# Performance work log

Hardware: AMD Instinct MI355X
Metric: run time of the kernel (lower is better)

## Reference

```python
import jax, jax.numpy as jnp
import numpy as np


def setup_inputs() -> dict:
    key = jax.random.key(0)
    k1, k2, k3, k4, k5, k6 = jax.random.split(key, 6)
    bs, sl, max_nw, dim_vtw, dim_hidden = 32, 1024, 16, 64, 128
    xw = jax.random.normal(k1, (bs, sl, max_nw, dim_vtw), dtype=jnp.float32)
    # xn: [bs, sl, ns+1]; only last column (word length, in [1, max_nw]) is used
    xn = jax.random.randint(k2, (bs, sl, 4), 1, max_nw + 1)
    s = 1.0 / np.sqrt(dim_hidden)
    W_ih = jax.random.uniform(k3, (4 * dim_hidden, dim_vtw), minval=-s, maxval=s, dtype=jnp.float32)
    W_hh = jax.random.uniform(k4, (4 * dim_hidden, dim_hidden), minval=-s, maxval=s, dtype=jnp.float32)
    b_ih = jax.random.uniform(k5, (4 * dim_hidden,), minval=-s, maxval=s, dtype=jnp.float32)
    b_hh = jax.random.uniform(k6, (4 * dim_hidden,), minval=-s, maxval=s, dtype=jnp.float32)
    return {"xw": xw, "xn": xn, "W_ih": W_ih, "W_hh": W_hh, "b_ih": b_ih, "b_hh": b_hh}


def reference(xw, xn, W_ih, W_hh, b_ih, b_hh):
    # Vectorized equivalent of the original per-group loop: run the LSTM over
    # the full max_nw timesteps for every (b, s) position (LSTM is causal, so
    # the hidden state after nw steps equals running only the first nw steps),
    # then gather h at t = length-1 per position.
    bs, sl, T, D = xw.shape
    H = W_hh.shape[1]
    N = bs * sl
    x = xw.reshape(N, T, D)
    lengths = xn[:, :, -1].reshape(N)
    # Precompute input contributions to all 4 gates: [T, N, 4H]
    x_gates = jnp.einsum('ntd,gd->tng', x, W_ih) + (b_ih + b_hh)

    def step(carry, xg):
        h, c = carry
        gates = xg + h @ W_hh.T  # [N, 4H]
        i, f, g, o = jnp.split(gates, 4, axis=-1)
        i = jax.nn.sigmoid(i)
        f = jax.nn.sigmoid(f)
        g = jnp.tanh(g)
        o = jax.nn.sigmoid(o)
        c = f * c + i * g
        h = o * jnp.tanh(c)
        return (h, c), h

    init = (jnp.zeros((N, H), xw.dtype), jnp.zeros((N, H), xw.dtype))
    _, hs = jax.lax.scan(step, init, x_gates)  # hs: [T, N, H]
    hs = jnp.swapaxes(hs, 0, 1)  # [N, T, H]
    idx = jnp.clip(lengths - 1, 0, T - 1)
    h_final = jnp.take_along_axis(hs, idx[:, None, None], axis=1)[:, 0]  # [N, H]
    return h_final.reshape(bs, sl, H)
```

## Files before the change

kernel.cpp:

```cpp
#include <hip/hip_runtime.h>
#include <math.h>

#define T_STEPS 16
#define DIM_X 64
#define DIM_H 128
#define DIM_K 192
#define NPACK 512
#define MSEQ 64
#define NTHREADS 512
#define LDK 200
#define PREP_THREADS 256
#define PACK_ITEMS (NPACK * DIM_K)
#define PACK_BLOCKS (PACK_ITEMS / PREP_THREADS)

typedef __attribute__((ext_vector_type(8))) short bf16x8;
typedef __attribute__((ext_vector_type(4))) float f32x4;

__device__ __forceinline__ float fsigmoid(float x) {
    return 1.0f / (1.0f + __expf(-x));
}
__device__ __forceinline__ float ftanh_(float x) {
    float a = fabsf(x);
    float e = __expf(2.0f * a);
    float r = 1.0f - 2.0f / (e + 1.0f);
    return copysignf(r, x);
}
__device__ __forceinline__ unsigned short bf16_rn(float x) {
    unsigned int b = __float_as_uint(x);
    b += 0x7FFFu + ((b >> 16) & 1u);
    return (unsigned short)(b >> 16);
}
__device__ __forceinline__ float bf16_to_f(unsigned short u) {
    return __uint_as_float(((unsigned int)u) << 16);
}

__global__ __launch_bounds__(PREP_THREADS)
void prep(const float* __restrict__ W_ih, const float* __restrict__ W_hh,
          const float* __restrict__ b_ih, const float* __restrict__ b_hh,
          const int* __restrict__ xn, int N,
          unsigned short* __restrict__ Whi, unsigned short* __restrict__ Wlo,
          float* __restrict__ bsum, int* __restrict__ list, int* __restrict__ ctr) {
    const int b = blockIdx.x;
    const int tid = threadIdx.x;
    if (b < PACK_BLOCKS) {
        int i = b * PREP_THREADS + tid;
        int p = i / DIM_K, k = i % DIM_K;
        int g = (p >> 4) & 3;
        int unit = ((p >> 6) << 4) + (p & 15);
        int r = g * DIM_H + unit;
        float v = (k < DIM_X) ? W_ih[r * DIM_X + k] : W_hh[r * DIM_H + (k - DIM_X)];
        unsigned short hi = bf16_rn(v);
        Whi[i] = hi;
        Wlo[i] = bf16_rn(v - bf16_to_f(hi));
        if (k == 0) bsum[p] = b_ih[r] + b_hh[r];
        return;
    }
    __shared__ int hist[T_STEPS], offs[T_STEPS], cur[T_STEPS];
    if (tid < T_STEPS) hist[tid] = 0;
    if (tid == 0) *ctr = 0;
    __syncthreads();
    for (int i = tid; i < N; i += PREP_THREADS) {
        int len = xn[i * 4 + 3];
        len = min(max(len, 1), T_STEPS);
        atomicAdd(&hist[len - 1], 1);
    }
    __syncthreads();
    if (tid == 0) {
        int acc = 0;
        for (int bb = T_STEPS - 1; bb >= 0; --bb) { offs[bb] = acc; acc += hist[bb]; }
    }
    __syncthreads();
    if (tid < T_STEPS) cur[tid] = offs[tid];
    __syncthreads();
    for (int i = tid; i < N; i += PREP_THREADS) {
        int len = xn[i * 4 + 3];
        len = min(max(len, 1), T_STEPS);
        int pos = atomicAdd(&cur[len - 1], 1);
        list[pos] = i;
    }
}

__global__ __launch_bounds__(NTHREADS)
void lstm_main(const float* __restrict__ xw, const int* __restrict__ xn,
               const unsigned short* __restrict__ Whi, const unsigned short* __restrict__ Wlo,
               const float* __restrict__ bsum, const int* __restrict__ list,
               int N, int* __restrict__ ctr, float* __restrict__ out)
{
    __shared__ unsigned short xh_hi[MSEQ][LDK];
    __shared__ unsigned short xh_lo[MSEQ][LDK];
    __shared__ int s_seq[MSEQ];
    __shared__ int s_len[MSEQ];
    __shared__ int s_chunk;

    const int tid = threadIdx.x;
    const int wv = tid >> 6;
    const int lane = tid & 63;
    const int lr = lane & 15;
    const int lh = lane >> 4;
    const int unit = (wv << 4) + lr;
    const int nchunks = (N + MSEQ - 1) / MSEQ;

    float bias[4];
#pragma unroll
    for (int g = 0; g < 4; ++g) bias[g] = bsum[(wv << 6) + (g << 4) + lr];
    const unsigned short* __restrict__ wbase_h = Whi + (size_t)(wv << 6) * DIM_K + (lh << 3);
    const unsigned short* __restrict__ wbase_l = Wlo + (size_t)(wv << 6) * DIM_K + (lh << 3);

    const int xsl = tid >> 3;
    const int xko = (tid & 7) << 3;

    while (true) {
        if (tid == 0) s_chunk = atomicAdd(ctr, 1);
        __syncthreads();
        const int chunk = s_chunk;
        if (chunk >= nchunks) break;

        if (tid < MSEQ) {
            int idx = chunk * MSEQ + tid;
            int seq = (idx < N) ? list[idx] : -1;
            s_seq[tid] = seq;
            int len = 0;
            if (seq >= 0) { len = xn[seq * 4 + 3]; len = min(max(len, 1), T_STEPS); }
            s_len[tid] = len;
        }
#pragma unroll
        for (int m = 0; m < 4; ++m)
#pragma unroll
            for (int j = 0; j < 4; ++j) {
                int s = (m << 4) + (lh << 2) + j;
                xh_hi[s][DIM_X + unit] = 0;
                xh_lo[s][DIM_X + unit] = 0;
            }
        __syncthreads();

        const int maxlen = s_len[0];
        int lenv[4][4];
#pragma unroll
        for (int m = 0; m < 4; ++m)
#pragma unroll
            for (int j = 0; j < 4; ++j) lenv[m][j] = s_len[(m << 4) + (lh << 2) + j];

        float c[4][4];
#pragma unroll
        for (int m = 0; m < 4; ++m)
#pragma unroll
            for (int j = 0; j < 4; ++j) c[m][j] = 0.0f;

        const long xseq = (long)max(s_seq[xsl], 0);

        {
            const float* xp = xw + ((size_t)xseq * T_STEPS + 0) * DIM_X + xko;
            f32x4 a = __builtin_nontemporal_load((const f32x4*)xp);
            f32x4 bq = __builtin_nontemporal_load((const f32x4*)(xp + 4));
            float xv[8] = {a[0], a[1], a[2], a[3], bq[0], bq[1], bq[2], bq[3]};
            bf16x8 hv, lv;
#pragma unroll
            for (int e = 0; e < 8; ++e) {
                unsigned short h = bf16_rn(xv[e]);
                hv[e] = (short)h;
                lv[e] = (short)bf16_rn(xv[e] - bf16_to_f(h));
            }
            *(bf16x8*)&xh_hi[xsl][xko] = hv;
            *(bf16x8*)&xh_lo[xsl][xko] = lv;
        }

        for (int t = 0; t < maxlen; ++t) {
            __syncthreads();

            f32x4 acc[4][4];
#pragma unroll
            for (int m = 0; m < 4; ++m)
#pragma unroll
                for (int g = 0; g < 4; ++g)
                    acc[m][g] = (f32x4){bias[g], bias[g], bias[g], bias[g]};

            for (int kc = 0; kc < 6; ++kc) {
                const int kb = kc << 5;
                bf16x8 ahi[4], alo[4];
#pragma unroll
                for (int m = 0; m < 4; ++m) {
                    ahi[m] = *(const bf16x8*)&xh_hi[(m << 4) + lr][kb + (lh << 3)];
                    alo[m] = *(const bf16x8*)&xh_lo[(m << 4) + lr][kb + (lh << 3)];
                }
                bf16x8 bhi[4], blo[4];
#pragma unroll
                for (int g = 0; g < 4; ++g) {
                    const size_t off = (size_t)((g << 4) + lr) * DIM_K + kb;
                    bhi[g] = *(const bf16x8*)(wbase_h + off);
                    blo[g] = *(const bf16x8*)(wbase_l + off);
                }
#pragma unroll
                for (int m = 0; m < 4; ++m)
#pragma unroll
                    for (int g = 0; g < 4; ++g) {
                        acc[m][g] = __builtin_amdgcn_mfma_f32_16x16x32_bf16(ahi[m], bhi[g], acc[m][g], 0, 0, 0);
                        acc[m][g] = __builtin_amdgcn_mfma_f32_16x16x32_bf16(alo[m], bhi[g], acc[m][g], 0, 0, 0);
                        acc[m][g] = __builtin_amdgcn_mfma_f32_16x16x32_bf16(ahi[m], blo[g], acc[m][g], 0, 0, 0);
                    }
            }

            const bool do_x = (t + 1 < maxlen);
            f32x4 xa, xb;
            if (do_x) {
                const float* xp = xw + ((size_t)xseq * T_STEPS + (t + 1)) * DIM_X + xko;
                xa = __builtin_nontemporal_load((const f32x4*)xp);
                xb = __builtin_nontemporal_load((const f32x4*)(xp + 4));
            }

            __syncthreads();

            if (do_x) {
                float xv[8] = {xa[0], xa[1], xa[2], xa[3], xb[0], xb[1], xb[2], xb[3]};
                bf16x8 hv, lv;
#pragma unroll
                for (int e = 0; e < 8; ++e) {
                    unsigned short h = bf16_rn(xv[e]);
                    hv[e] = (short)h;
                    lv[e] = (short)bf16_rn(xv[e] - bf16_to_f(h));
                }
                *(bf16x8*)&xh_hi[xsl][xko] = hv;
                *(bf16x8*)&xh_lo[xsl][xko] = lv;
            }

#pragma unroll
            for (int m = 0; m < 4; ++m)
#pragma unroll
                for (int j = 0; j < 4; ++j) {
                    float iv = fsigmoid(acc[m][0][j]);
                    float fv = fsigmoid(acc[m][1][j]);
                    float gv = ftanh_(acc[m][2][j]);
                    float ov = fsigmoid(acc[m][3][j]);
                    float cv = fv * c[m][j] + iv * gv;
                    c[m][j] = cv;
                    float hv = ov * ftanh_(cv);
                    int s = (m << 4) + (lh << 2) + j;
                    unsigned short hh = bf16_rn(hv);
                    xh_hi[s][DIM_X + unit] = hh;
                    xh_lo[s][DIM_X + unit] = bf16_rn(hv - bf16_to_f(hh));
                    if (t == lenv[m][j] - 1) {
                        int gs = s_seq[s];
                        if (gs >= 0)
                            __builtin_nontemporal_store(hv, &out[(size_t)gs * DIM_H + unit]);
                    }
                }
        }
    }
}

extern "C" void kernel_launch(void* const* d_in, const int* in_sizes, int n_in,
                              void* d_out, int out_size, void* d_ws, size_t ws_size,
                              hipStream_t stream) {
    const float* xw   = (const float*)d_in[0];
    const int*   xn   = (const int*)d_in[1];
    const float* W_ih = (const float*)d_in[2];
    const float* W_hh = (const float*)d_in[3];
    const float* b_ih = (const float*)d_in[4];
    const float* b_hh = (const float*)d_in[5];
    float* out = (float*)d_out;

    const int N = in_sizes[0] / (T_STEPS * DIM_X);

    char* ws = (char*)d_ws;
    unsigned short* Whi  = (unsigned short*)ws;
    unsigned short* Wlo  = (unsigned short*)(ws + 196608);
    float*          bsum = (float*)(ws + 393216);
    int*            ctr  = (int*)(ws + 395264);
    int*            list = (int*)(ws + 395328);

    prep<<<PACK_BLOCKS + 1, PREP_THREADS, 0, stream>>>(W_ih, W_hh, b_ih, b_hh, xn, N,
                                                       Whi, Wlo, bsum, list, ctr);

    const int nchunks = (N + MSEQ - 1) / MSEQ;
    const int nblocks = min(256, nchunks);
    lstm_main<<<nblocks, NTHREADS, 0, stream>>>(xw, xn, Whi, Wlo, bsum, list, N, ctr, out);
}
```

Measured before the change: 560.2 us.

## Repack LSTM weights into lane-contiguous fragment layout and unroll k-loop

Reorders the bf16 hi/lo split weights into one buffer laid out per wave, k-chunk, gate and hi/lo pair, so each lane's 8-element fragment is contiguous and a wave's loads coalesce into 1KB runs. This replaces strided row-major reads of the global weights, which are issued every timestep. It also fully unrolls the k-chunk loop and sets launch bounds to two blocks per SM. The extra unrolling and occupancy hint may raise register pressure or cause spills.

```diff
diff --git a/kernel.cpp b/kernel.cpp
--- a/kernel.cpp
+++ b/kernel.cpp
@@ -5,13 +5,16 @@
 #define DIM_X 64
 #define DIM_H 128
 #define DIM_K 192
-#define NPACK 512
 #define MSEQ 64
 #define NTHREADS 512
 #define LDK 200
 #define PREP_THREADS 256
-#define PACK_ITEMS (NPACK * DIM_K)
-#define PACK_BLOCKS (PACK_ITEMS / PREP_THREADS)
+#define WF_STRIDE_PAIR 512
+#define WF_STRIDE_G    1024
+#define WF_STRIDE_KC   4096
+#define WF_STRIDE_W    24576
+#define WF_TOTAL       196608
+#define PACK_BLOCKS (WF_TOTAL / PREP_THREADS)
 
 typedef __attribute__((ext_vector_type(8))) short bf16x8;
 typedef __attribute__((ext_vector_type(4))) float f32x4;
@@ -38,21 +41,29 @@
 void prep(const float* __restrict__ W_ih, const float* __restrict__ W_hh,
           const float* __restrict__ b_ih, const float* __restrict__ b_hh,
           const int* __restrict__ xn, int N,
-          unsigned short* __restrict__ Whi, unsigned short* __restrict__ Wlo,
-          float* __restrict__ bsum, int* __restrict__ list, int* __restrict__ ctr) {
+          unsigned short* __restrict__ Wf, float* __restrict__ bsum,
+          int* __restrict__ list, int* __restrict__ ctr) {
     const int b = blockIdx.x;
     const int tid = threadIdx.x;
     if (b < PACK_BLOCKS) {
         int i = b * PREP_THREADS + tid;
-        int p = i / DIM_K, k = i % DIM_K;
-        int g = (p >> 4) & 3;
-        int unit = ((p >> 6) << 4) + (p & 15);
-        int r = g * DIM_H + unit;
-        float v = (k < DIM_X) ? W_ih[r * DIM_X + k] : W_hh[r * DIM_H + (k - DIM_X)];
+        int w    = i / WF_STRIDE_W;
+        int r1   = i % WF_STRIDE_W;
+        int kc   = r1 / WF_STRIDE_KC;
+        int r2   = r1 % WF_STRIDE_KC;
+        int g    = r2 / WF_STRIDE_G;
+        int r3   = r2 % WF_STRIDE_G;
+        int pair = r3 / WF_STRIDE_PAIR;
+        int r4   = r3 % WF_STRIDE_PAIR;
+        int lane = r4 >> 3;
+        int e    = r4 & 7;
+        int row = g * DIM_H + w * 16 + (lane & 15);
+        int k   = kc * 32 + (lane >> 4) * 8 + e;
+        float v = (k < DIM_X) ? W_ih[row * DIM_X + k] : W_hh[row * DIM_H + (k - DIM_X)];
         unsigned short hi = bf16_rn(v);
-        Whi[i] = hi;
-        Wlo[i] = bf16_rn(v - bf16_to_f(hi));
-        if (k == 0) bsum[p] = b_ih[r] + b_hh[r];
+        Wf[i] = pair ? bf16_rn(v - bf16_to_f(hi)) : hi;
+        if (kc == 0 && pair == 0 && lane < 16 && e == 0)
+            bsum[w * 64 + g * 16 + lane] = b_ih[row] + b_hh[row];
         return;
     }
     __shared__ int hist[T_STEPS], offs[T_STEPS], cur[T_STEPS];
@@ -80,9 +91,9 @@
     }
 }
 
-__global__ __launch_bounds__(NTHREADS)
+__global__ __launch_bounds__(NTHREADS, 2)
 void lstm_main(const float* __restrict__ xw, const int* __restrict__ xn,
-               const unsigned short* __restrict__ Whi, const unsigned short* __restrict__ Wlo,
+               const unsigned short* __restrict__ Wf,
                const float* __restrict__ bsum, const int* __restrict__ list,
                int N, int* __restrict__ ctr, float* __restrict__ out)
 {
@@ -103,8 +114,7 @@
     float bias[4];
 #pragma unroll
     for (int g = 0; g < 4; ++g) bias[g] = bsum[(wv << 6) + (g << 4) + lr];
-    const unsigned short* __restrict__ wbase_h = Whi + (size_t)(wv << 6) * DIM_K + (lh << 3);
-    const unsigned short* __restrict__ wbase_l = Wlo + (size_t)(wv << 6) * DIM_K + (lh << 3);
+    const unsigned short* __restrict__ wfb = Wf + (size_t)wv * WF_STRIDE_W + (lane << 3);
 
     const int xsl = tid >> 3;
     const int xko = (tid & 7) << 3;
@@ -174,6 +184,7 @@
                 for (int g = 0; g < 4; ++g)
                     acc[m][g] = (f32x4){bias[g], bias[g], bias[g], bias[g]};
 
+#pragma unroll
             for (int kc = 0; kc < 6; ++kc) {
                 const int kb = kc << 5;
                 bf16x8 ahi[4], alo[4];
@@ -185,9 +196,9 @@
                 bf16x8 bhi[4], blo[4];
 #pragma unroll
                 for (int g = 0; g < 4; ++g) {
-                    const size_t off = (size_t)((g << 4) + lr) * DIM_K + kb;
-                    bhi[g] = *(const bf16x8*)(wbase_h + off);
-                    blo[g] = *(const bf16x8*)(wbase_l + off);
+                    const unsigned short* p = wfb + kc * WF_STRIDE_KC + g * WF_STRIDE_G;
+                    bhi[g] = *(const bf16x8*)p;
+                    blo[g] = *(const bf16x8*)(p + WF_STRIDE_PAIR);
                 }
 #pragma unroll
                 for (int m = 0; m < 4; ++m)
@@ -261,16 +272,15 @@
     const int N = in_sizes[0] / (T_STEPS * DIM_X);
 
     char* ws = (char*)d_ws;
-    unsigned short* Whi  = (unsigned short*)ws;
-    unsigned short* Wlo  = (unsigned short*)(ws + 196608);
+    unsigned short* Wf   = (unsigned short*)ws;
     float*          bsum = (float*)(ws + 393216);
     int*            ctr  = (int*)(ws + 395264);
     int*            list = (int*)(ws + 395328);
 
     prep<<<PACK_BLOCKS + 1, PREP_THREADS, 0, stream>>>(W_ih, W_hh, b_ih, b_hh, xn, N,
-                                                       Whi, Wlo, bsum, list, ctr);
+                                                       Wf, bsum, list, ctr);
 
     const int nchunks = (N + MSEQ - 1) / MSEQ;
     const int nblocks = min(256, nchunks);
-    lstm_main<<<nblocks, NTHREADS, 0, stream>>>(xw, xn, Whi, Wlo, bsum, list, N, ctr, out);
-}
+    lstm_main<<<nblocks, NTHREADS, 0, stream>>>(xw, xn, Wf, bsum, list, N, ctr, out);
+}
```

Result: no change. 565.7 us (+1.0%).
